# Optimization experiments

Hardware: AMD Instinct MI355X
Metric: run time of the kernel (lower is better)

## Reference

```python
import jax, jax.numpy as jnp
import numpy as np

H = 2048          # hidden_size
I = 8192          # intermediate_size (shared expert)
E = 32            # num_experts
K = 4             # num_experts_per_tok
M = 1408          # moe_intermediate_size
B, S = 2, 1024


def setup_inputs() -> dict:
    key = jax.random.key(0)
    ks = jax.random.split(key, 7)
    scale = 0.02
    return {
        "hidden_states": jax.random.normal(ks[0], (B, S, H), dtype=jnp.float32),
        "gate_w": jax.random.normal(ks[1], (H, E), dtype=jnp.float32) * scale,
        "w1": jax.random.normal(ks[2], (E, H, M), dtype=jnp.float32) * scale,  # expert up-proj
        "w2": jax.random.normal(ks[3], (E, M, H), dtype=jnp.float32) * scale,  # expert down-proj
        "ws1": jax.random.normal(ks[4], (H, I), dtype=jnp.float32) * scale,    # shared up-proj
        "ws2": jax.random.normal(ks[5], (I, H), dtype=jnp.float32) * scale,    # shared down-proj
    }


def reference(hidden_states, gate_w, w1, w2, ws1, ws2):
    b, s, h = hidden_states.shape
    x = hidden_states.reshape(-1, h)                      # [T, H]

    # shared expert: Linear -> SiLU -> Linear
    shared = jax.nn.silu(x @ ws1) @ ws2                   # [T, H]

    # router: top-k logits, softmax over the k selected logits
    router_logits = x @ gate_w                            # [T, E]
    top_vals, top_idx = jax.lax.top_k(router_logits, K)   # [T, K]
    routing_weights = jax.nn.softmax(top_vals, axis=-1)   # [T, K]

    # combine weights: scatter top-k weights into dense [T, E]
    cw = (jax.nn.one_hot(top_idx, E, dtype=x.dtype)
          * routing_weights[..., None]).sum(axis=1)       # [T, E]

    # expert FFNs (dense over experts, weighted combine)
    a = jax.nn.silu(jnp.einsum('th,ehm->tem', x, w1))     # [T, E, M]
    expert_out = jnp.einsum('tem,emh,te->th', a, w2, cw)  # [T, H]

    output = (shared + expert_out).reshape(b, s, h)
    return output, router_logits.reshape(b, s, E)
```

## Files before the change

### kernel.cpp

```cpp
#include <hip/hip_runtime.h>

#define H_ 2048
#define E_ 32
#define KSEL 4
#define M_ 1408
#define I_ 8192
#define T_ 2048

typedef __bf16 bf16;
typedef bf16 bf16x8 __attribute__((ext_vector_type(8)));
typedef float f32x4 __attribute__((ext_vector_type(4)));
typedef unsigned short u16x8 __attribute__((ext_vector_type(8)));
typedef unsigned int u32x4 __attribute__((ext_vector_type(4)));

static __device__ __forceinline__ unsigned short bfb(float f) {
  return __builtin_bit_cast(unsigned short, (bf16)f);
}

static __device__ __forceinline__ void gload_lds16(const void* g, void* l) {
  __builtin_amdgcn_global_load_lds((const __attribute__((address_space(1))) void*)g,
                                   (__attribute__((address_space(3))) void*)l, 16, 0, 0);
}

static __device__ __forceinline__ float silu_f(float v) {
  return v / (1.f + __expf(-v));
}

static __device__ __forceinline__ void wave_argmax(float& v, int& vi) {
  #pragma unroll
  for (int off = 32; off >= 1; off >>= 1) {
    float ov = __shfl_xor(v, off);
    int   oi = __shfl_xor(vi, off);
    if (ov > v || (ov == v && oi < vi)) { v = ov; vi = oi; }
  }
}

__global__ __launch_bounds__(256) void prep_k(float* __restrict__ out, int* __restrict__ counts) {
  size_t i = ((size_t)blockIdx.x * 256 + threadIdx.x) * 4;
  *(float4*)(out + i) = make_float4(0.f, 0.f, 0.f, 0.f);
  if (blockIdx.x == 0 && threadIdx.x < E_) counts[threadIdx.x] = 0;
}

__global__ __launch_bounds__(256) void cvt_k(const float* __restrict__ x, unsigned short* __restrict__ xb) {
  size_t i = ((size_t)blockIdx.x * 256 + threadIdx.x) * 8;
  float4 a = *(const float4*)(x + i);
  float4 b = *(const float4*)(x + i + 4);
  u16x8 o;
  o[0]=bfb(a.x); o[1]=bfb(a.y); o[2]=bfb(a.z); o[3]=bfb(a.w);
  o[4]=bfb(b.x); o[5]=bfb(b.y); o[6]=bfb(b.z); o[7]=bfb(b.w);
  *(u16x8*)(xb + i) = o;
}

__global__ __launch_bounds__(64) void router_k(const float* __restrict__ x, const float* __restrict__ gw,
                                               float* __restrict__ logits, int* __restrict__ counts,
                                               int* __restrict__ tlist, float* __restrict__ wlist) {
  int t = blockIdx.x;
  int l = threadIdx.x;
  int e = l & 31;
  int half = l >> 5;
  const float* xr = x + (size_t)t * H_ + half * (H_/2);
  const float* g  = gw + (size_t)(half * (H_/2)) * E_ + e;
  float a0=0.f, a1=0.f, a2=0.f, a3=0.f;
  for (int h = 0; h < H_/2; h += 4) {
    a0 = fmaf(xr[h],   g[(size_t)h*E_],     a0);
    a1 = fmaf(xr[h+1], g[(size_t)(h+1)*E_], a1);
    a2 = fmaf(xr[h+2], g[(size_t)(h+2)*E_], a2);
    a3 = fmaf(xr[h+3], g[(size_t)(h+3)*E_], a3);
  }
  float acc = (a0+a1)+(a2+a3);
  acc += __shfl_xor(acc, 32);
  if (l < E_) logits[(size_t)t*E_ + l] = acc;

  float cur = (l < E_) ? acc : -INFINITY;
  int myidx = (l < E_) ? e : 1000;
  float tv0,tv1,tv2,tv3; int ti0,ti1,ti2,ti3;
  { float v=cur; int vi=myidx; wave_argmax(v,vi); tv0=v; ti0=vi; if (myidx==vi) cur=-INFINITY; }
  { float v=cur; int vi=myidx; wave_argmax(v,vi); tv1=v; ti1=vi; if (myidx==vi) cur=-INFINITY; }
  { float v=cur; int vi=myidx; wave_argmax(v,vi); tv2=v; ti2=vi; if (myidx==vi) cur=-INFINITY; }
  { float v=cur; int vi=myidx; wave_argmax(v,vi); tv3=v; ti3=vi; }
  float w0 = 1.f;
  float w1 = __expf(tv1 - tv0);
  float w2 = __expf(tv2 - tv0);
  float w3 = __expf(tv3 - tv0);
  float inv = 1.f / (w0+w1+w2+w3);
  if (l < KSEL) {
    float myw = ((l==0)?w0:(l==1)?w1:(l==2)?w2:w3) * inv;
    int   myi = ((l==0)?ti0:(l==1)?ti1:(l==2)?ti2:ti3);
    int pos = atomicAdd(&counts[myi], 1);
    tlist[myi*T_ + pos] = (t << 2) | l;
    wlist[myi*T_ + pos] = myw;
  }
}

template<int MODE, int KDIM, int NDIM, int ASTR, int KSPLIT>
__global__ __launch_bounds__(256) void gemm_k(
    const bf16* __restrict__ A, const float* __restrict__ Bf,
    bf16* __restrict__ Cb, float* __restrict__ Cf,
    const int* __restrict__ tlist, const float* __restrict__ wlist,
    const int* __restrict__ counts)
{
  __shared__ __align__(16) char smem[16384];
  char* As = smem;
  char* Bs = smem + 8192;
  const int tid = threadIdx.x;

  int mt, nt, e = 0, kz = 0;
  int nrows = T_;
  const int* lst = nullptr;
  const float* Bp = Bf;
  if constexpr (MODE == 2 || MODE == 3) {
    constexpr int NT = NDIM / 128;
    e  = blockIdx.x / NT;
    nt = blockIdx.x % NT;
    mt = blockIdx.y;
    nrows = counts[e];
    if (mt * 128 >= nrows) return;
    lst = tlist + e*T_;
    Bp = Bf + (size_t)e * ((size_t)KDIM * NDIM);
  } else {
    constexpr int NWG = 16 * (NDIM / 128);
    constexpr int CPX = NWG / 8;
    int id = blockIdx.x;
    int lg = (id & 7) * CPX + (id >> 3);
    mt = lg & 15;
    nt = lg >> 4;
    if constexpr (KSPLIT > 1) kz = blockIdx.z;
  }
  const int mrow0 = mt*128, ncol0 = nt*128;

  const bf16* abase[2];
  int aoffs[2];
  #pragma unroll
  for (int hh = 0; hh < 2; ++hh) {
    int lidx = hh*256 + tid;
    int row  = lidx >> 2;
    int slog = (lidx & 3) ^ (row & 3);
    aoffs[hh] = slog * 8;
    int ri = mrow0 + row;
    if constexpr (MODE == 2) {
      int tt = (ri < nrows) ? (lst[ri] >> 2) : 0;
      abase[hh] = A + (size_t)tt * ASTR;
    } else if constexpr (MODE == 3) {
      int ar = (ri < nrows) ? lst[ri] : 0;
      abase[hh] = A + (size_t)ar * ASTR;
    } else {
      abase[hh] = A + (size_t)ri * ASTR;
    }
  }

  const int bn = tid & 127;
  const int bh = tid >> 7;
  const float* bsrc0 = Bp + (size_t)(bh * 16) * NDIM + ncol0 + bn;
  char* bdst0 = Bs + (bh*2)*2048 + bn*16;

  const int l  = tid & 63;
  const int wv = tid >> 6;
  const int wr = wv >> 1, wc = wv & 1;
  const int ss = l >> 4;

  f32x4 acc[4][4] = {};

  constexpr int ITERS = KDIM / 32 / KSPLIT;
  const int kt0 = kz * ITERS;

  for (int kt = kt0; kt < kt0 + ITERS; ++kt) {
    const int k0 = kt * 32;
    __syncthreads();
    #pragma unroll
    for (int hh = 0; hh < 2; ++hh)
      gload_lds16(abase[hh] + k0 + aoffs[hh], As + (hh*256 + tid)*16);
    {
      const float* bs = bsrc0 + (size_t)k0 * NDIM;
      float bv[16];
      #pragma unroll
      for (int j = 0; j < 16; ++j) bv[j] = bs[(size_t)j * NDIM];
      unsigned pk[8];
      #pragma unroll
      for (int jj = 0; jj < 8; ++jj)
        pk[jj] = (unsigned)bfb(bv[2*jj]) | ((unsigned)bfb(bv[2*jj+1]) << 16);
      u32x4 lo, hi;
      lo[0]=pk[0]; lo[1]=pk[1]; lo[2]=pk[2]; lo[3]=pk[3];
      hi[0]=pk[4]; hi[1]=pk[5]; hi[2]=pk[6]; hi[3]=pk[7];
      *(u32x4*)(bdst0)        = lo;
      *(u32x4*)(bdst0 + 2048) = hi;
    }
    __syncthreads();
    bf16x8 af[4], bfr[4];
    #pragma unroll
    for (int mf = 0; mf < 4; ++mf) {
      int r = wr*64 + mf*16 + (l & 15);
      af[mf] = *(const bf16x8*)(As + r*64 + ((ss ^ (r & 3)) << 4));
    }
    #pragma unroll
    for (int nf = 0; nf < 4; ++nf) {
      int c = wc*64 + nf*16 + (l & 15);
      bfr[nf] = *(const bf16x8*)(Bs + ss*2048 + c*16);
    }
    #pragma unroll
    for (int mf = 0; mf < 4; ++mf)
      #pragma unroll
      for (int nf = 0; nf < 4; ++nf)
        acc[mf][nf] = __builtin_amdgcn_mfma_f32_16x16x32_bf16(af[mf], bfr[nf], acc[mf][nf], 0, 0, 0);
  }

  #pragma unroll
  for (int mf = 0; mf < 4; ++mf) {
    #pragma unroll
    for (int j = 0; j < 4; ++j) {
      const int rloc = wr*64 + mf*16 + (l >> 4)*4 + j;
      const int grow = mrow0 + rloc;
      if constexpr (MODE == 0) {
        #pragma unroll
        for (int nf = 0; nf < 4; ++nf) {
          int col = ncol0 + wc*64 + nf*16 + (l & 15);
          Cb[(size_t)grow * NDIM + col] = (bf16)silu_f(acc[mf][nf][j]);
        }
      } else if constexpr (MODE == 1) {
        #pragma unroll
        for (int nf = 0; nf < 4; ++nf) {
          int col = ncol0 + wc*64 + nf*16 + (l & 15);
          atomicAdd(Cf + (size_t)grow * NDIM + col, acc[mf][nf][j]);
        }
      } else if constexpr (MODE == 2) {
        if (grow < nrows) {
          int entry = lst[grow];
          float wg = wlist[e*T_ + grow];
          #pragma unroll
          for (int nf = 0; nf < 4; ++nf) {
            int col = ncol0 + wc*64 + nf*16 + (l & 15);
            Cb[(size_t)entry * NDIM + col] = (bf16)(silu_f(acc[mf][nf][j]) * wg);
          }
        }
      } else {
        if (grow < nrows) {
          int entry = lst[grow];
          int tt = entry >> 2;
          #pragma unroll
          for (int nf = 0; nf < 4; ++nf) {
            int col = ncol0 + wc*64 + nf*16 + (l & 15);
            atomicAdd(Cf + (size_t)tt * H_ + col, acc[mf][nf][j]);
          }
        }
      }
    }
  }
}

extern "C" void kernel_launch(void* const* d_in, const int* in_sizes, int n_in,
                              void* d_out, int out_size, void* d_ws, size_t ws_size,
                              hipStream_t stream) {
  const float* x   = (const float*)d_in[0];
  const float* gw  = (const float*)d_in[1];
  const float* w1  = (const float*)d_in[2];
  const float* w2  = (const float*)d_in[3];
  const float* ws1 = (const float*)d_in[4];
  const float* ws2 = (const float*)d_in[5];
  float* out    = (float*)d_out;
  float* logits = out + (size_t)T_ * H_;

  char* ws = (char*)d_ws;
  const size_t off_xb   = 0;
  const size_t off_y1   = off_xb  + (size_t)T_ * H_ * 2;
  const size_t off_act  = off_y1  + (size_t)T_ * I_ * 2;
  const size_t off_cnt  = off_act + (size_t)T_ * 4 * M_ * 2;
  const size_t off_tl   = off_cnt + 256;
  const size_t off_wl   = off_tl  + (size_t)E_ * T_ * 4;

  const bf16* xb = (const bf16*)(ws + off_xb);
  bf16* y1  = (bf16*)(ws + off_y1);
  bf16* act = (bf16*)(ws + off_act);
  int*  counts = (int*)(ws + off_cnt);
  int*  tlist  = (int*)(ws + off_tl);
  float* wlist = (float*)(ws + off_wl);

  prep_k<<<4096, 256, 0, stream>>>(out, counts);
  router_k<<<T_, 64, 0, stream>>>(x, gw, logits, counts, tlist, wlist);
  cvt_k<<<2048, 256, 0, stream>>>(x, (unsigned short*)(ws + off_xb));

  gemm_k<0, 2048, 8192, 2048, 1><<<dim3(1024), 256, 0, stream>>>(
      xb, ws1, y1, nullptr, nullptr, nullptr, nullptr);
  gemm_k<1, 8192, 2048, 8192, 4><<<dim3(256, 1, 4), 256, 0, stream>>>(
      y1, ws2, nullptr, out, nullptr, nullptr, nullptr);
  gemm_k<2, 2048, 1408, 2048, 1><<<dim3(11*E_, 16), 256, 0, stream>>>(
      xb, w1, act, nullptr, tlist, wlist, counts);
  gemm_k<3, 1408, 2048, 1408, 1><<<dim3(16*E_, 16), 256, 0, stream>>>(
      act, w2, nullptr, out, tlist, nullptr, counts);
}
```

Before: 857.3 us.

## Prefetch B tile into registers across K iterations and split-K expert down-proj

Restructures the GEMM K-loop into a 2-unrolled, register double-buffered pipeline, so the fp32 B loads for the next K step are issued before the MFMA work of the current step. This is meant to hide global-load latency behind compute. It also enables split-K (2) for the expert down-projection, which raises the number of workgroups. The costs are more atomic adds to the output and higher register pressure from the extra 16-float buffer.

```diff
diff --git a/kernel.cpp b/kernel.cpp
--- a/kernel.cpp
+++ b/kernel.cpp
@@ -117,6 +117,7 @@
     if (mt * 128 >= nrows) return;
     lst = tlist + e*T_;
     Bp = Bf + (size_t)e * ((size_t)KDIM * NDIM);
+    if constexpr (KSPLIT > 1) kz = blockIdx.z;
   } else {
     constexpr int NWG = 16 * (NDIM / 128);
     constexpr int CPX = NWG / 8;
@@ -161,47 +162,85 @@
   f32x4 acc[4][4] = {};
 
   constexpr int ITERS = KDIM / 32 / KSPLIT;
+  static_assert(ITERS % 2 == 0, "K-loop is 2-unrolled");
   const int kt0 = kz * ITERS;
-
-  for (int kt = kt0; kt < kt0 + ITERS; ++kt) {
-    const int k0 = kt * 32;
+  const int ktend = kt0 + ITERS;
+
+  float vA0,vA1,vA2,vA3,vA4,vA5,vA6,vA7,vA8,vA9,vA10,vA11,vA12,vA13,vA14,vA15;
+  float vB0,vB1,vB2,vB3,vB4,vB5,vB6,vB7,vB8,vB9,vB10,vB11,vB12,vB13,vB14,vB15;
+
+#define LOADB(P, KT) do {                                            \
+    const float* bs_ = bsrc0 + (size_t)((KT) * 32) * NDIM;           \
+    P##0 = bs_[0];            P##1 = bs_[(size_t)1*NDIM];            \
+    P##2 = bs_[(size_t)2*NDIM];  P##3 = bs_[(size_t)3*NDIM];         \
+    P##4 = bs_[(size_t)4*NDIM];  P##5 = bs_[(size_t)5*NDIM];         \
+    P##6 = bs_[(size_t)6*NDIM];  P##7 = bs_[(size_t)7*NDIM];         \
+    P##8 = bs_[(size_t)8*NDIM];  P##9 = bs_[(size_t)9*NDIM];         \
+    P##10 = bs_[(size_t)10*NDIM]; P##11 = bs_[(size_t)11*NDIM];      \
+    P##12 = bs_[(size_t)12*NDIM]; P##13 = bs_[(size_t)13*NDIM];      \
+    P##14 = bs_[(size_t)14*NDIM]; P##15 = bs_[(size_t)15*NDIM];      \
+  } while (0)
+
+#define WRITEB(P) do {                                               \
+    u32x4 lo_, hi_;                                                  \
+    lo_[0] = (unsigned)bfb(P##0)  | ((unsigned)bfb(P##1)  << 16);    \
+    lo_[1] = (unsigned)bfb(P##2)  | ((unsigned)bfb(P##3)  << 16);    \
+    lo_[2] = (unsigned)bfb(P##4)  | ((unsigned)bfb(P##5)  << 16);    \
+    lo_[3] = (unsigned)bfb(P##6)  | ((unsigned)bfb(P##7)  << 16);    \
+    hi_[0] = (unsigned)bfb(P##8)  | ((unsigned)bfb(P##9)  << 16);    \
+    hi_[1] = (unsigned)bfb(P##10) | ((unsigned)bfb(P##11) << 16);    \
+    hi_[2] = (unsigned)bfb(P##12) | ((unsigned)bfb(P##13) << 16);    \
+    hi_[3] = (unsigned)bfb(P##14) | ((unsigned)bfb(P##15) << 16);    \
+    *(u32x4*)(bdst0)        = lo_;                                   \
+    *(u32x4*)(bdst0 + 2048) = hi_;                                   \
+  } while (0)
+
+#define MFMA_PHASE(KT) do {                                          \
+    bf16x8 af[4], bfr[4];                                            \
+    _Pragma("unroll")                                                \
+    for (int mf = 0; mf < 4; ++mf) {                                 \
+      int r = wr*64 + mf*16 + (l & 15);                              \
+      af[mf] = *(const bf16x8*)(As + r*64 + ((ss ^ (r & 3)) << 4));  \
+    }                                                                \
+    _Pragma("unroll")                                                \
+    for (int nf = 0; nf < 4; ++nf) {                                 \
+      int c = wc*64 + nf*16 + (l & 15);                              \
+      bfr[nf] = *(const bf16x8*)(Bs + ss*2048 + c*16);               \
+    }                                                                \
+    _Pragma("unroll")                                                \
+    for (int mf = 0; mf < 4; ++mf)                                   \
+      _Pragma("unroll")                                              \
+      for (int nf = 0; nf < 4; ++nf)                                 \
+        acc[mf][nf] = __builtin_amdgcn_mfma_f32_16x16x32_bf16(af[mf], bfr[nf], acc[mf][nf], 0, 0, 0); \
+  } while (0)
+
+#define ADMA(KT) do {                                                \
+    _Pragma("unroll")                                                \
+    for (int hh = 0; hh < 2; ++hh)                                   \
+      gload_lds16(abase[hh] + (KT)*32 + aoffs[hh], As + (hh*256 + tid)*16); \
+  } while (0)
+
+  LOADB(vA, kt0);
+  for (int kt = kt0; kt < ktend; kt += 2) {
     __syncthreads();
-    #pragma unroll
-    for (int hh = 0; hh < 2; ++hh)
-      gload_lds16(abase[hh] + k0 + aoffs[hh], As + (hh*256 + tid)*16);
-    {
-      const float* bs = bsrc0 + (size_t)k0 * NDIM;
-      float bv[16];
-      #pragma unroll
-      for (int j = 0; j < 16; ++j) bv[j] = bs[(size_t)j * NDIM];
-      unsigned pk[8];
-      #pragma unroll
-      for (int jj = 0; jj < 8; ++jj)
-        pk[jj] = (unsigned)bfb(bv[2*jj]) | ((unsigned)bfb(bv[2*jj+1]) << 16);
-      u32x4 lo, hi;
-      lo[0]=pk[0]; lo[1]=pk[1]; lo[2]=pk[2]; lo[3]=pk[3];
-      hi[0]=pk[4]; hi[1]=pk[5]; hi[2]=pk[6]; hi[3]=pk[7];
-      *(u32x4*)(bdst0)        = lo;
-      *(u32x4*)(bdst0 + 2048) = hi;
-    }
+    ADMA(kt);
+    WRITEB(vA);
     __syncthreads();
-    bf16x8 af[4], bfr[4];
-    #pragma unroll
-    for (int mf = 0; mf < 4; ++mf) {
-      int r = wr*64 + mf*16 + (l & 15);
-      af[mf] = *(const bf16x8*)(As + r*64 + ((ss ^ (r & 3)) << 4));
-    }
-    #pragma unroll
-    for (int nf = 0; nf < 4; ++nf) {
-      int c = wc*64 + nf*16 + (l & 15);
-      bfr[nf] = *(const bf16x8*)(Bs + ss*2048 + c*16);
-    }
-    #pragma unroll
-    for (int mf = 0; mf < 4; ++mf)
-      #pragma unroll
-      for (int nf = 0; nf < 4; ++nf)
-        acc[mf][nf] = __builtin_amdgcn_mfma_f32_16x16x32_bf16(af[mf], bfr[nf], acc[mf][nf], 0, 0, 0);
-  }
+    LOADB(vB, kt + 1);
+    MFMA_PHASE(kt);
+
+    __syncthreads();
+    ADMA(kt + 1);
+    WRITEB(vB);
+    __syncthreads();
+    if (kt + 2 < ktend) LOADB(vA, kt + 2);
+    MFMA_PHASE(kt + 1);
+  }
+
+#undef LOADB
+#undef WRITEB
+#undef MFMA_PHASE
+#undef ADMA
 
   #pragma unroll
   for (int mf = 0; mf < 4; ++mf) {
@@ -283,6 +322,6 @@
       y1, ws2, nullptr, out, nullptr, nullptr, nullptr);
   gemm_k<2, 2048, 1408, 2048, 1><<<dim3(11*E_, 16), 256, 0, stream>>>(
       xb, w1, act, nullptr, tlist, wlist, counts);
-  gemm_k<3, 1408, 2048, 1408, 1><<<dim3(16*E_, 16), 256, 0, stream>>>(
+  gemm_k<3, 1408, 2048, 1408, 2><<<dim3(16*E_, 16, 2), 256, 0, stream>>>(
       act, w2, nullptr, out, tlist, nullptr, counts);
 }
```

New measurement: 854.0 us. Within noise of the previous version (-0.4%).
